# Optimization experiments

Measured on AMD Instinct MI355X. Metric: run time of the kernel, lower is better.

Reference implementation:

```python
import jax, jax.numpy as jnp
import numpy as np

D_MODEL = 768
N_HEAD = 12
D_FF = 3072
EPS = 1e-5


def _layer_norm(x, w, b):
    mu = jnp.mean(x, axis=-1, keepdims=True)
    var = jnp.mean(jnp.square(x - mu), axis=-1, keepdims=True)
    return (x - mu) * jax.lax.rsqrt(var + EPS) * w + b


def setup_inputs() -> dict:
    key = jax.random.key(0)
    ks = jax.random.split(key, 8)
    B, S, D = 2, 4096, D_MODEL
    s_in = 1.0 / np.sqrt(D)
    s_ff = 1.0 / np.sqrt(D_FF)
    return {
        "src": jax.random.normal(ks[0], (B, S, D), jnp.float32),
        "w_qkv": jax.random.uniform(ks[1], (3 * D, D), jnp.float32, -s_in, s_in),
        "b_qkv": jnp.zeros((3 * D,), jnp.float32),
        "w_out": jax.random.uniform(ks[2], (D, D), jnp.float32, -s_in, s_in),
        "b_out": jnp.zeros((D,), jnp.float32),
        "w1": jax.random.uniform(ks[3], (D_FF, D), jnp.float32, -s_in, s_in),
        "b1": jnp.zeros((D_FF,), jnp.float32),
        "w2": jax.random.uniform(ks[4], (D, D_FF), jnp.float32, -s_ff, s_ff),
        "b2": jnp.zeros((D,), jnp.float32),
        "ln1_w": jnp.ones((D,), jnp.float32),
        "ln1_b": jnp.zeros((D,), jnp.float32),
        "ln2_w": jnp.ones((D,), jnp.float32),
        "ln2_b": jnp.zeros((D,), jnp.float32),
    }


def reference(src, w_qkv, b_qkv, w_out, b_out, w1, b1, w2, b2,
              ln1_w, ln1_b, ln2_w, ln2_b):
    B, S, D = src.shape
    H, dh = N_HEAD, D // N_HEAD
    # fused QKV projection: [B,S,3D]
    qkv = jnp.einsum('bsd,ed->bse', src, w_qkv) + b_qkv
    q, k, v = jnp.split(qkv, 3, axis=-1)
    q = q.reshape(B, S, H, dh)
    k = k.reshape(B, S, H, dh)
    v = v.reshape(B, S, H, dh)
    scale = 1.0 / np.sqrt(dh)
    scores = jnp.einsum('bqhd,bkhd->bhqk', q, k) * scale  # [B,H,S,S]
    attn = jax.nn.softmax(scores, axis=-1)
    ctx = jnp.einsum('bhqk,bkhd->bqhd', attn, v).reshape(B, S, D)
    attn_out = jnp.einsum('bsd,ed->bse', ctx, w_out) + b_out
    # post-norm residual (norm_first=False), dropout inactive in eval
    x = _layer_norm(src + attn_out, ln1_w, ln1_b)
    h = jax.nn.relu(jnp.einsum('bsd,fd->bsf', x, w1) + b1)
    ffn = jnp.einsum('bsf,df->bsd', h, w2) + b2
    return _layer_norm(x + ffn, ln2_w, ln2_b)
```

## Files before the change

### kernel.cpp

```cpp
#include <hip/hip_runtime.h>
#include <hip/hip_bf16.h>

typedef __hip_bfloat16 bf16;
typedef __attribute__((ext_vector_type(8))) short s16x8;
typedef __attribute__((ext_vector_type(4))) float f32x4;

#define MFMA16x16x32(A, B, C) __builtin_amdgcn_mfma_f32_16x16x32_bf16((A), (B), (C), 0, 0, 0)

__device__ __forceinline__ void async_copy16(const bf16* g, bf16* l) {
  __builtin_amdgcn_global_load_lds(
      (const __attribute__((address_space(1))) void*)g,
      (__attribute__((address_space(3))) void*)l, 16, 0, 0);
}

__device__ __forceinline__ float swz_x16(float x) {
  return __int_as_float(__builtin_amdgcn_ds_swizzle(__float_as_int(x), 0x401f));
}

__device__ __forceinline__ int SW(int row, int chunk) {
  return row * 64 + (((chunk) ^ (row & 7)) << 3);
}

__global__ __launch_bounds__(256)
void cast_f2b_kernel(const float* __restrict__ in, bf16* __restrict__ out, int n) {
  const int i = (blockIdx.x * 256 + threadIdx.x) * 4;
  if (i < n) {
    const float4 f = *(const float4*)(in + i);
    out[i + 0] = (bf16)f.x; out[i + 1] = (bf16)f.y;
    out[i + 2] = (bf16)f.z; out[i + 3] = (bf16)f.w;
  }
}

template <int RELU, int VT, int ACCUM, typename OutT>
__global__ __launch_bounds__(256)
void gemm_bt_kernel(const bf16* __restrict__ A, const bf16* __restrict__ B,
                    const float* __restrict__ bias, OutT* __restrict__ C,
                    int N, int K, int ldb) {
  __shared__ __align__(16) bf16 As[128 * 32];
  __shared__ __align__(16) bf16 Bs[128 * 32];

  const int t = threadIdx.x;
  const int lane = t & 63;
  const int wave = t >> 6;
  const int wm = (wave >> 1) << 6;
  const int wn = (wave & 1) << 6;
  const int col16 = lane & 15;
  const int quad = lane >> 4;
  const int bm = blockIdx.x;
  const int bn = blockIdx.y;

  const bf16* Ag = A + (size_t)(bm * 128 + (t >> 2)) * K + (t & 3) * 8;
  const bf16* Bg = B + (size_t)(bn * 128 + (t >> 2)) * ldb + (t & 3) * 8;
  bf16* Asd = As + t * 8;
  bf16* Bsd = Bs + t * 8;

  f32x4 acc[4][4] = {};

  for (int k0 = 0; k0 < K; k0 += 32) {
    __syncthreads();
    async_copy16(Ag + k0, Asd);
    async_copy16(Ag + (size_t)64 * K + k0, Asd + 2048);
    async_copy16(Bg + k0, Bsd);
    async_copy16(Bg + (size_t)64 * ldb + k0, Bsd + 2048);
    asm volatile("s_waitcnt vmcnt(0)" ::: "memory");
    __syncthreads();

    s16x8 af[4], bfr[4];
#pragma unroll
    for (int i = 0; i < 4; i++)
      af[i] = *(const s16x8*)(As + (wm + i * 16 + col16) * 32 + quad * 8);
#pragma unroll
    for (int j = 0; j < 4; j++)
      bfr[j] = *(const s16x8*)(Bs + (wn + j * 16 + col16) * 32 + quad * 8);
#pragma unroll
    for (int i = 0; i < 4; i++)
#pragma unroll
      for (int j = 0; j < 4; j++)
        acc[i][j] = MFMA16x16x32(af[i], bfr[j], acc[i][j]);
  }

  const int row0 = bm * 128 + wm + quad * 4;
  const int col0 = bn * 128 + wn + col16;
#pragma unroll
  for (int j = 0; j < 4; j++) {
    const int col = col0 + j * 16;
    const float bv = ACCUM ? 0.0f : bias[col];
#pragma unroll
    for (int i = 0; i < 4; i++) {
#pragma unroll
      for (int r = 0; r < 4; r++) {
        float v = acc[i][j][r] + bv;
        if (RELU) v = fmaxf(v, 0.0f);
        const int row = row0 + i * 16 + r;
        if (VT) {
          ((bf16*)C)[(size_t)((row >> 12) * 12 + (col >> 6)) * 262144 +
                     (col & 63) * 4096 + (row & 4095)] = (bf16)v;
        } else {
          const size_t idx = (size_t)row * N + col;
          if (ACCUM) v += ((const float*)C)[idx];
          C[idx] = (OutT)v;
        }
      }
    }
  }
}

__global__ __launch_bounds__(256)
void attn_kernel(const bf16* __restrict__ QK, const bf16* __restrict__ Vt,
                 bf16* __restrict__ Opart, float* __restrict__ lbuf) {
  __shared__ __align__(16) bf16 Ks[64 * 64];
  __shared__ __align__(16) bf16 Vs[64 * 64];
  __shared__ __align__(16) bf16 Ps[4][32 * 64];

  const int t = threadIdx.x, lane = t & 63, wave = t >> 6;
  const int col16 = lane & 15, quad = lane >> 4;
  const int b = blockIdx.z, h = blockIdx.y;
  const int ks = blockIdx.x >> 5;
  const int qblk = blockIdx.x & 31;
  const int qw0 = qblk * 128 + wave * 32;

  s16x8 bq[2][2];
#pragma unroll
  for (int qt = 0; qt < 2; qt++)
#pragma unroll
    for (int s = 0; s < 2; s++) {
      union { s16x8 v; bf16 hh[8]; } u;
      u.v = *(const s16x8*)(QK + (size_t)(b * 4096 + qw0 + qt * 16 + col16) * 1536 +
                            h * 64 + s * 32 + quad * 8);
#pragma unroll
      for (int e = 0; e < 8; e++) u.hh[e] = (bf16)((float)u.hh[e] * 0.18033688f);
      bq[qt][s] = u.v;
    }

  const bf16* kbase = QK + (size_t)(b * 4096) * 1536 + 768 + h * 64;
  const bf16* vbase = Vt + (size_t)(b * 12 + h) * 262144;
  const int srow = t >> 2;
  const int cch = t & 3;

  f32x4 o[4][2] = {};
  float l_[2] = {0.0f, 0.0f};
  bf16* pw = &Ps[wave][0];

  const int kend = ks * 2048 + 2048;
  for (int k0 = ks * 2048; k0 < kend; k0 += 64) {
    const s16x8 kc0 = *(const s16x8*)(kbase + (size_t)(k0 + srow) * 1536 + cch * 8);
    const s16x8 kc1 = *(const s16x8*)(kbase + (size_t)(k0 + srow) * 1536 + cch * 8 + 32);
    const s16x8 vc0 = *(const s16x8*)(vbase + (size_t)srow * 4096 + k0 + cch * 8);
    const s16x8 vc1 = *(const s16x8*)(vbase + (size_t)srow * 4096 + k0 + cch * 8 + 32);
    __syncthreads();
    *(s16x8*)(Ks + SW(srow, cch)) = kc0;
    *(s16x8*)(Ks + SW(srow, cch + 4)) = kc1;
    *(s16x8*)(Vs + SW(srow, cch)) = vc0;
    *(s16x8*)(Vs + SW(srow, cch + 4)) = vc1;
    __syncthreads();

    f32x4 st[4][2] = {};
#pragma unroll
    for (int s = 0; s < 2; s++) {
      s16x8 ak[4];
#pragma unroll
      for (int kt = 0; kt < 4; kt++)
        ak[kt] = *(const s16x8*)(Ks + SW(kt * 16 + col16, s * 4 + quad));
#pragma unroll
      for (int kt = 0; kt < 4; kt++)
#pragma unroll
        for (int qt = 0; qt < 2; qt++)
          st[kt][qt] = MFMA16x16x32(ak[kt], bq[qt][s], st[kt][qt]);
    }

#pragma unroll
    for (int qt = 0; qt < 2; qt++) {
#pragma unroll
      for (int kt = 0; kt < 4; kt++) {
        union { unsigned long long u; bf16 hh[4]; } pk;
#pragma unroll
        for (int r = 0; r < 4; r++) {
          const float p = exp2f(st[kt][qt][r]);
          l_[qt] += p;
          pk.hh[r] = (bf16)p;
        }
        *(unsigned long long*)(pw + (qt * 16 + col16) * 64 +
                               (((kt * 2 + (quad >> 1)) ^ (col16 & 7)) << 3) +
                               (quad & 1) * 4) = pk.u;
      }
    }
    asm volatile("s_waitcnt lgkmcnt(0)" ::: "memory");

#pragma unroll
    for (int s = 0; s < 2; s++) {
      s16x8 bp[2];
#pragma unroll
      for (int qt = 0; qt < 2; qt++)
        bp[qt] = *(const s16x8*)(pw + SW(qt * 16 + col16, s * 4 + quad));
#pragma unroll
      for (int dt = 0; dt < 4; dt++) {
        const s16x8 av = *(const s16x8*)(Vs + SW(dt * 16 + col16, s * 4 + quad));
#pragma unroll
        for (int qt = 0; qt < 2; qt++)
          o[dt][qt] = MFMA16x16x32(av, bp[qt], o[dt][qt]);
      }
    }
  }

  float lsum[2];
#pragma unroll
  for (int qt = 0; qt < 2; qt++) {
    float l = l_[qt];
    l += swz_x16(l);
    l += __shfl_xor(l, 32, 64);
    lsum[qt] = l;
  }
  if (lane < 16) {
#pragma unroll
    for (int qt = 0; qt < 2; qt++)
      lbuf[(size_t)ks * 98304 + (size_t)(b * 4096 + qw0 + qt * 16 + lane) * 12 + h] = lsum[qt];
  }

#pragma unroll
  for (int qt = 0; qt < 2; qt++)
#pragma unroll
    for (int dt = 0; dt < 4; dt++)
#pragma unroll
      for (int r = 0; r < 4; r++)
        pw[(qt * 16 + col16) * 64 + (((dt * 2 + (quad >> 1)) ^ (col16 & 7)) << 3) +
           (quad & 1) * 4 + r] = (bf16)(o[dt][qt][r]);
  asm volatile("s_waitcnt lgkmcnt(0)" ::: "memory");
  const int qrow = lane >> 1, chalf = (lane & 1) * 4;
  bf16* dst = Opart + (size_t)ks * 6291456 +
              (size_t)(b * 4096 + qw0 + qrow) * 768 + h * 64 + chalf * 8;
#pragma unroll
  for (int i = 0; i < 4; i++)
    *(s16x8*)(dst + i * 8) = *(const s16x8*)(pw + SW(qrow, chalf + i));
}

__global__ __launch_bounds__(256)
void attn_combine_kernel(const bf16* __restrict__ Opart,
                         const float* __restrict__ lbuf,
                         bf16* __restrict__ ctx) {
  const int i = blockIdx.x * 256 + threadIdx.x;
  const int row = i / 96, c8 = i % 96;
  const int h = c8 >> 3;
  const float inv = 1.0f / (lbuf[(size_t)row * 12 + h] +
                            lbuf[98304 + (size_t)row * 12 + h]);
  union { s16x8 v; bf16 hh[8]; } ua, ub, uo;
  ua.v = *(const s16x8*)(Opart + (size_t)row * 768 + c8 * 8);
  ub.v = *(const s16x8*)(Opart + 6291456 + (size_t)row * 768 + c8 * 8);
#pragma unroll
  for (int j = 0; j < 8; j++)
    uo.hh[j] = (bf16)(((float)ua.hh[j] + (float)ub.hh[j]) * inv);
  *(s16x8*)(ctx + (size_t)row * 768 + c8 * 8) = uo.v;
}

__global__ __launch_bounds__(256)
void add_ln_b_kernel(const float* __restrict__ X, const float* __restrict__ Y,
                     const float* __restrict__ w, const float* __restrict__ b,
                     bf16* __restrict__ out) {
  const int row = blockIdx.x * 4 + (threadIdx.x >> 6);
  const int lane = threadIdx.x & 63;
  const float* x = X + (size_t)row * 768;
  const float* y = Y + (size_t)row * 768;
  float v[12];
  float s = 0.0f;
#pragma unroll
  for (int i = 0; i < 3; i++) {
    const int c = lane * 4 + i * 256;
    const float4 xf = *(const float4*)(x + c);
    const float4 yf = *(const float4*)(y + c);
    v[i * 4 + 0] = xf.x + yf.x; v[i * 4 + 1] = xf.y + yf.y;
    v[i * 4 + 2] = xf.z + yf.z; v[i * 4 + 3] = xf.w + yf.w;
    s += v[i * 4] + v[i * 4 + 1] + v[i * 4 + 2] + v[i * 4 + 3];
  }
#pragma unroll
  for (int off = 32; off > 0; off >>= 1) s += __shfl_xor(s, off, 64);
  const float mu = s * (1.0f / 768.0f);
  float var = 0.0f;
#pragma unroll
  for (int i = 0; i < 12; i++) { const float d = v[i] - mu; var += d * d; }
#pragma unroll
  for (int off = 32; off > 0; off >>= 1) var += __shfl_xor(var, off, 64);
  const float rs = rsqrtf(var * (1.0f / 768.0f) + 1e-5f);
#pragma unroll
  for (int i = 0; i < 12; i++) {
    const int c = lane * 4 + (i >> 2) * 256 + (i & 3);
    out[(size_t)row * 768 + c] = (bf16)((v[i] - mu) * rs * w[c] + b[c]);
  }
}

__global__ __launch_bounds__(256)
void add_ln_f_kernel(const bf16* __restrict__ X, const float* __restrict__ Y,
                     const float* __restrict__ w, const float* __restrict__ b,
                     float* __restrict__ out) {
  const int row = blockIdx.x * 4 + (threadIdx.x >> 6);
  const int lane = threadIdx.x & 63;
  const bf16* x = X + (size_t)row * 768;
  const float* y = Y + (size_t)row * 768;
  float v[12];
  float s = 0.0f;
#pragma unroll
  for (int i = 0; i < 3; i++) {
    const int c = lane * 4 + i * 256;
    const float4 yf = *(const float4*)(y + c);
    v[i * 4 + 0] = (float)x[c + 0] + yf.x; v[i * 4 + 1] = (float)x[c + 1] + yf.y;
    v[i * 4 + 2] = (float)x[c + 2] + yf.z; v[i * 4 + 3] = (float)x[c + 3] + yf.w;
    s += v[i * 4] + v[i * 4 + 1] + v[i * 4 + 2] + v[i * 4 + 3];
  }
#pragma unroll
  for (int off = 32; off > 0; off >>= 1) s += __shfl_xor(s, off, 64);
  const float mu = s * (1.0f / 768.0f);
  float var = 0.0f;
#pragma unroll
  for (int i = 0; i < 12; i++) { const float d = v[i] - mu; var += d * d; }
#pragma unroll
  for (int off = 32; off > 0; off >>= 1) var += __shfl_xor(var, off, 64);
  const float rs = rsqrtf(var * (1.0f / 768.0f) + 1e-5f);
#pragma unroll
  for (int i = 0; i < 12; i++) {
    const int c = lane * 4 + (i >> 2) * 256 + (i & 3);
    out[(size_t)row * 768 + c] = (v[i] - mu) * rs * w[c] + b[c];
  }
}

extern "C" void kernel_launch(void* const* d_in, const int* in_sizes, int n_in,
                              void* d_out, int out_size, void* d_ws, size_t ws_size,
                              hipStream_t stream) {
  (void)in_sizes; (void)n_in; (void)out_size; (void)ws_size;
  const float* src   = (const float*)d_in[0];
  const float* w_qkv = (const float*)d_in[1];
  const float* b_qkv = (const float*)d_in[2];
  const float* w_out = (const float*)d_in[3];
  const float* b_out = (const float*)d_in[4];
  const float* w1    = (const float*)d_in[5];
  const float* b1    = (const float*)d_in[6];
  const float* w2    = (const float*)d_in[7];
  const float* b2    = (const float*)d_in[8];
  const float* ln1w  = (const float*)d_in[9];
  const float* ln1b  = (const float*)d_in[10];
  const float* ln2w  = (const float*)d_in[11];
  const float* ln2b  = (const float*)d_in[12];
  float* out = (float*)d_out;

  char* ws = (char*)d_ws;
  bf16* wqkvb = (bf16*)ws;
  bf16* woutb = (bf16*)(ws + 3538944);
  bf16* w1b   = (bf16*)(ws + 4718592);
  bf16* w2b   = (bf16*)(ws + 9437184);
  bf16* srcb  = (bf16*)(ws + 14155776);
  bf16* QK    = (bf16*)(ws + 26738688);
  bf16* Vt    = (bf16*)(ws + 51904512);
  bf16* Opart = (bf16*)d_out;
  float* lbuf = (float*)ws;
  bf16* ctx   = (bf16*)(ws + 14155776);
  float* attn_out = (float*)(ws + 26738688);
  bf16* x1b   = (bf16*)(ws + 51904512);
  bf16* hbuf  = (bf16*)(ws + 14155776);
  float* ffn  = out;

  cast_f2b_kernel<<<1728, 256, 0, stream>>>(w_qkv, wqkvb, 2304 * 768);
  cast_f2b_kernel<<<576,  256, 0, stream>>>(w_out, woutb, 768 * 768);
  cast_f2b_kernel<<<2304, 256, 0, stream>>>(w1, w1b, 3072 * 768);
  cast_f2b_kernel<<<2304, 256, 0, stream>>>(w2, w2b, 768 * 3072);
  cast_f2b_kernel<<<6144, 256, 0, stream>>>(src, srcb, 8192 * 768);

  gemm_bt_kernel<0, 0, 0, bf16><<<dim3(64, 12), 256, 0, stream>>>(
      srcb, wqkvb, b_qkv, QK, 1536, 768, 768);
  gemm_bt_kernel<0, 1, 0, bf16><<<dim3(64, 6), 256, 0, stream>>>(
      srcb, wqkvb + (size_t)1536 * 768, b_qkv + 1536, Vt, 768, 768, 768);
  attn_kernel<<<dim3(64, 12, 2), 256, 0, stream>>>(QK, Vt, Opart, lbuf);
  attn_combine_kernel<<<3072, 256, 0, stream>>>(Opart, lbuf, ctx);
  gemm_bt_kernel<0, 0, 0, float><<<dim3(64, 6), 256, 0, stream>>>(
      ctx, woutb, b_out, attn_out, 768, 768, 768);
  add_ln_b_kernel<<<2048, 256, 0, stream>>>(src, attn_out, ln1w, ln1b, x1b);
  for (int c = 0; c < 2; c++) {
    gemm_bt_kernel<1, 0, 0, bf16><<<dim3(64, 12), 256, 0, stream>>>(
        x1b, w1b + (size_t)c * 1536 * 768, b1 + c * 1536, hbuf, 1536, 768, 768);
    if (c == 0)
      gemm_bt_kernel<0, 0, 0, float><<<dim3(64, 6), 256, 0, stream>>>(
          hbuf, w2b + c * 1536, b2, ffn, 768, 1536, 3072);
    else
      gemm_bt_kernel<0, 0, 1, float><<<dim3(64, 6), 256, 0, stream>>>(
          hbuf, w2b + c * 1536, b2, ffn, 768, 1536, 3072);
  }
  add_ln_f_kernel<<<2048, 256, 0, stream>>>(x1b, ffn, ln2w, ln2b, out);
}
```

Baseline: 530.3 us.

## Load K/V tiles directly into registers and compute softmax row sums via MFMA

The attention kernel no longer stages K and V tiles through shared memory with two block-wide barriers per iteration. Each wave now loads its MFMA operand fragments straight from global memory. The softmax denominator is accumulated with an extra MFMA against a vector of bf16 ones instead of scalar adds plus a cross-lane reduction, and exp2f is replaced by the hardware exp2 intrinsic. This removes LDS traffic and syncs, but each of the four waves now re-reads the same K/V data from global/L2 instead of sharing it. The row sums are also now taken from the bf16-rounded probabilities.

```diff
diff --git a/kernel.cpp b/kernel.cpp
--- a/kernel.cpp
+++ b/kernel.cpp
@@ -11,10 +11,6 @@
   __builtin_amdgcn_global_load_lds(
       (const __attribute__((address_space(1))) void*)g,
       (__attribute__((address_space(3))) void*)l, 16, 0, 0);
-}
-
-__device__ __forceinline__ float swz_x16(float x) {
-  return __int_as_float(__builtin_amdgcn_ds_swizzle(__float_as_int(x), 0x401f));
 }
 
 __device__ __forceinline__ int SW(int row, int chunk) {
@@ -108,8 +104,6 @@
 __global__ __launch_bounds__(256)
 void attn_kernel(const bf16* __restrict__ QK, const bf16* __restrict__ Vt,
                  bf16* __restrict__ Opart, float* __restrict__ lbuf) {
-  __shared__ __align__(16) bf16 Ks[64 * 64];
-  __shared__ __align__(16) bf16 Vs[64 * 64];
   __shared__ __align__(16) bf16 Ps[4][32 * 64];
 
   const int t = threadIdx.x, lane = t & 63, wave = t >> 6;
@@ -132,41 +126,42 @@
       bq[qt][s] = u.v;
     }
 
-  const bf16* kbase = QK + (size_t)(b * 4096) * 1536 + 768 + h * 64;
-  const bf16* vbase = Vt + (size_t)(b * 12 + h) * 262144;
-  const int srow = t >> 2;
-  const int cch = t & 3;
+  union { s16x8 v; short s_[8]; } uo1;
+#pragma unroll
+  for (int e = 0; e < 8; e++) uo1.s_[e] = (short)0x3F80;
+  const s16x8 aones = uo1.v;
+
+  const bf16* kb = QK + (size_t)(b * 4096 + col16) * 1536 + 768 + h * 64 + quad * 8;
+  const bf16* vb = Vt + (size_t)(b * 12 + h) * 262144 + (size_t)col16 * 4096 + quad * 8;
 
   f32x4 o[4][2] = {};
-  float l_[2] = {0.0f, 0.0f};
+  f32x4 lacc[2] = {};
   bf16* pw = &Ps[wave][0];
 
   const int kend = ks * 2048 + 2048;
   for (int k0 = ks * 2048; k0 < kend; k0 += 64) {
-    const s16x8 kc0 = *(const s16x8*)(kbase + (size_t)(k0 + srow) * 1536 + cch * 8);
-    const s16x8 kc1 = *(const s16x8*)(kbase + (size_t)(k0 + srow) * 1536 + cch * 8 + 32);
-    const s16x8 vc0 = *(const s16x8*)(vbase + (size_t)srow * 4096 + k0 + cch * 8);
-    const s16x8 vc1 = *(const s16x8*)(vbase + (size_t)srow * 4096 + k0 + cch * 8 + 32);
-    __syncthreads();
-    *(s16x8*)(Ks + SW(srow, cch)) = kc0;
-    *(s16x8*)(Ks + SW(srow, cch + 4)) = kc1;
-    *(s16x8*)(Vs + SW(srow, cch)) = vc0;
-    *(s16x8*)(Vs + SW(srow, cch + 4)) = vc1;
-    __syncthreads();
+    s16x8 akr[2][4];
+#pragma unroll
+    for (int s = 0; s < 2; s++)
+#pragma unroll
+      for (int kt = 0; kt < 4; kt++)
+        akr[s][kt] = *(const s16x8*)(kb + (size_t)(k0 + kt * 16) * 1536 + s * 32);
 
     f32x4 st[4][2] = {};
 #pragma unroll
-    for (int s = 0; s < 2; s++) {
-      s16x8 ak[4];
+    for (int s = 0; s < 2; s++)
 #pragma unroll
       for (int kt = 0; kt < 4; kt++)
-        ak[kt] = *(const s16x8*)(Ks + SW(kt * 16 + col16, s * 4 + quad));
-#pragma unroll
-      for (int kt = 0; kt < 4; kt++)
 #pragma unroll
         for (int qt = 0; qt < 2; qt++)
-          st[kt][qt] = MFMA16x16x32(ak[kt], bq[qt][s], st[kt][qt]);
-    }
+          st[kt][qt] = MFMA16x16x32(akr[s][kt], bq[qt][s], st[kt][qt]);
+
+    s16x8 avr[2][4];
+#pragma unroll
+    for (int s = 0; s < 2; s++)
+#pragma unroll
+      for (int dt = 0; dt < 4; dt++)
+        avr[s][dt] = *(const s16x8*)(vb + (size_t)dt * 16 * 4096 + k0 + s * 32);
 
 #pragma unroll
     for (int qt = 0; qt < 2; qt++) {
@@ -174,11 +169,8 @@
       for (int kt = 0; kt < 4; kt++) {
         union { unsigned long long u; bf16 hh[4]; } pk;
 #pragma unroll
-        for (int r = 0; r < 4; r++) {
-          const float p = exp2f(st[kt][qt][r]);
-          l_[qt] += p;
-          pk.hh[r] = (bf16)p;
-        }
+        for (int r = 0; r < 4; r++)
+          pk.hh[r] = (bf16)__builtin_amdgcn_exp2f(st[kt][qt][r]);
         *(unsigned long long*)(pw + (qt * 16 + col16) * 64 +
                                (((kt * 2 + (quad >> 1)) ^ (col16 & 7)) << 3) +
                                (quad & 1) * 4) = pk.u;
@@ -193,27 +185,22 @@
       for (int qt = 0; qt < 2; qt++)
         bp[qt] = *(const s16x8*)(pw + SW(qt * 16 + col16, s * 4 + quad));
 #pragma unroll
+      for (int qt = 0; qt < 2; qt++)
+        lacc[qt] = MFMA16x16x32(aones, bp[qt], lacc[qt]);
+#pragma unroll
       for (int dt = 0; dt < 4; dt++) {
-        const s16x8 av = *(const s16x8*)(Vs + SW(dt * 16 + col16, s * 4 + quad));
 #pragma unroll
         for (int qt = 0; qt < 2; qt++)
-          o[dt][qt] = MFMA16x16x32(av, bp[qt], o[dt][qt]);
+          o[dt][qt] = MFMA16x16x32(avr[s][dt], bp[qt], o[dt][qt]);
       }
     }
   }
 
-  float lsum[2];
-#pragma unroll
-  for (int qt = 0; qt < 2; qt++) {
-    float l = l_[qt];
-    l += swz_x16(l);
-    l += __shfl_xor(l, 32, 64);
-    lsum[qt] = l;
-  }
   if (lane < 16) {
 #pragma unroll
     for (int qt = 0; qt < 2; qt++)
-      lbuf[(size_t)ks * 98304 + (size_t)(b * 4096 + qw0 + qt * 16 + lane) * 12 + h] = lsum[qt];
+      lbuf[(size_t)ks * 98304 + (size_t)(b * 4096 + qw0 + qt * 16 + lane) * 12 + h] =
+          lacc[qt][0];
   }
 
 #pragma unroll
```

New measurement: 714.2 us. 34.7% more time.
